# Optimization experiments

Hardware: AMD Instinct MI355X
Metric: run time of the kernel (lower is better)

Reference implementation:

```python
import jax, jax.numpy as jnp
import numpy as np

L_MAX = 3
MP_SCALING = 0.1
E = 640000
N_ATOMS = 20000
K = 32


def setup_inputs() -> dict:
    key = jax.random.key(0)
    k1, k2, k3, k4, k5 = jax.random.split(key, 5)
    sh = jax.random.normal(k1, (E, (L_MAX + 1) ** 2), dtype=jnp.float32)
    radial_basis = jax.random.normal(k2, (E, L_MAX + 1, K), dtype=jnp.float32)
    center_embedding = jax.random.normal(k3, (N_ATOMS, K), dtype=jnp.float32)
    centers = jax.random.randint(k4, (E,), 0, N_ATOMS, dtype=jnp.int32)
    neighbors = jax.random.randint(k5, (E,), 0, N_ATOMS, dtype=jnp.int32)
    return {
        "sh": sh,
        "radial_basis": radial_basis,
        "center_embedding": center_embedding,
        "centers": centers,
        "neighbors": neighbors,
        "n_atoms": N_ATOMS,
    }


def reference(sh, radial_basis, center_embedding, centers, neighbors, n_atoms):
    # Gather neighbor embeddings once: [E, K]
    emb_n = center_embedding[neighbors]
    blocks = []
    off = 0
    for l in range(L_MAX + 1):
        m = 2 * l + 1
        sh_l = sh[:, off:off + m]            # [E, m]
        off += m
        rb_l = radial_basis[:, l, :]          # [E, K]
        # edge-wise product sh * radial * gathered embedding: [E, m, K]
        src = sh_l[:, :, None] * (rb_l * emb_n)[:, None, :]
        # scatter-add over center atoms -> per-atom density [n_atoms, m, K]
        dens_l = jax.ops.segment_sum(src, centers, num_segments=n_atoms)
        blocks.append(dens_l * MP_SCALING)
    # concatenate per-l blocks along the component axis: [n_atoms, sum(2l+1)=16, K]
    return jnp.concatenate(blocks, axis=1)
```

## Files before the change

kernel.cpp:

```cpp
#include <hip/hip_runtime.h>

#define KDIM 32
#define CAP 160

__global__ void scatter_slots_kernel(const int* __restrict__ centers,
                                     const int* __restrict__ neighbors,
                                     int* __restrict__ cursor,
                                     int2* __restrict__ recs, int n) {
    int i = blockIdx.x * blockDim.x + threadIdx.x;
    if (i < n) {
        int c  = centers[i];
        int nn = neighbors[i];
        int pos = atomicAdd(&cursor[c], 1);
        if (pos < CAP) recs[(size_t)c * CAP + pos] = make_int2(i, nn);
    }
}


#define EDGE_BODY(EB, RP, SHP)                                            \
    {                                                                     \
        float t0 = RP[0 * KDIM + k] * EB;                                 \
        float t1 = RP[1 * KDIM + k] * EB;                                 \
        float t2 = RP[2 * KDIM + k] * EB;                                 \
        float t3 = RP[3 * KDIM + k] * EB;                                 \
        float4 sA = SHP[0];                                               \
        float4 sB = SHP[1];                                               \
        float c0 = hb ? t2 : t0;                                          \
        float c1 = hb ? t3 : t1;                                          \
        float c2 = hb ? t3 : t2;                                          \
        a0 += sA.x * c0;                                                  \
        a1 += sA.y * c1;                                                  \
        a2 += sA.z * c1;                                                  \
        a3 += sA.w * c1;                                                  \
        a4 += sB.x * c2;                                                  \
        a5 += sB.y * c2;                                                  \
        a6 += sB.z * c2;                                                  \
        a7 += sB.w * c2;                                                  \
    }

__global__ __launch_bounds__(256) void imp_main_kernel(
    const float* __restrict__ sh, const float* __restrict__ rb,
    const float* __restrict__ emb, const int2* __restrict__ recs,
    const int* __restrict__ cursor, float* __restrict__ out, int n_atoms) {
    int wid  = threadIdx.x >> 6;
    int aib  = wid >> 1;
    int half = wid & 1;
    int atom = blockIdx.x * 2 + aib;
    int lane = threadIdx.x & 63;
    int k = lane & 31;
    int h = lane >> 5;
    bool hb = (h != 0);

    __shared__ float red[2][8 * 64];

    float a0 = 0.f, a1 = 0.f, a2 = 0.f, a3 = 0.f;
    float a4 = 0.f, a5 = 0.f, a6 = 0.f, a7 = 0.f;

    bool valid = (atom < n_atoms);
    int i = 0, lim = 0;
    size_t base = (size_t)atom * CAP;
    if (valid) {
        int cnt = cursor[atom];
        if (cnt > CAP) cnt = CAP;
        int mid = (cnt + 1) >> 1;
        i   = half ? mid : 0;
        lim = half ? cnt : mid;
    }
    const int2* rbase = recs + base;

    for (; i + 4 <= lim; i += 4) {
        int2 r0 = rbase[i + 0];
        int2 r1 = rbase[i + 1];
        int2 r2 = rbase[i + 2];
        int2 r3 = rbase[i + 3];
        int e0 = __builtin_amdgcn_readfirstlane(r0.x);
        int n0 = __builtin_amdgcn_readfirstlane(r0.y);
        int e1 = __builtin_amdgcn_readfirstlane(r1.x);
        int n1 = __builtin_amdgcn_readfirstlane(r1.y);
        int e2 = __builtin_amdgcn_readfirstlane(r2.x);
        int n2 = __builtin_amdgcn_readfirstlane(r2.y);
        int e3 = __builtin_amdgcn_readfirstlane(r3.x);
        int n3 = __builtin_amdgcn_readfirstlane(r3.y);

        float eb0 = emb[(size_t)n0 * KDIM + k];
        float eb1 = emb[(size_t)n1 * KDIM + k];
        float eb2 = emb[(size_t)n2 * KDIM + k];
        float eb3 = emb[(size_t)n3 * KDIM + k];

        const float* rp0 = rb + (size_t)e0 * (4 * KDIM);
        const float* rp1 = rb + (size_t)e1 * (4 * KDIM);
        const float* rp2 = rb + (size_t)e2 * (4 * KDIM);
        const float* rp3 = rb + (size_t)e3 * (4 * KDIM);

        const float4* sp0 = (const float4*)(sh + (size_t)e0 * 16 + 8 * h);
        const float4* sp1 = (const float4*)(sh + (size_t)e1 * 16 + 8 * h);
        const float4* sp2 = (const float4*)(sh + (size_t)e2 * 16 + 8 * h);
        const float4* sp3 = (const float4*)(sh + (size_t)e3 * 16 + 8 * h);

        EDGE_BODY(eb0, rp0, sp0)
        EDGE_BODY(eb1, rp1, sp1)
        EDGE_BODY(eb2, rp2, sp2)
        EDGE_BODY(eb3, rp3, sp3)
    }
    for (; i < lim; i++) {
        int2 r0 = rbase[i];
        int e0 = __builtin_amdgcn_readfirstlane(r0.x);
        int n0 = __builtin_amdgcn_readfirstlane(r0.y);
        float eb0 = emb[(size_t)n0 * KDIM + k];
        const float* rp0 = rb + (size_t)e0 * (4 * KDIM);
        const float4* sp0 = (const float4*)(sh + (size_t)e0 * 16 + 8 * h);
        EDGE_BODY(eb0, rp0, sp0)
    }

    if (half) {
        float* rp = &red[aib][0];
        rp[0 * 64 + lane] = a0;
        rp[1 * 64 + lane] = a1;
        rp[2 * 64 + lane] = a2;
        rp[3 * 64 + lane] = a3;
        rp[4 * 64 + lane] = a4;
        rp[5 * 64 + lane] = a5;
        rp[6 * 64 + lane] = a6;
        rp[7 * 64 + lane] = a7;
    }
    __syncthreads();
    if (!half && valid) {
        const float* rp = &red[aib][0];
        a0 += rp[0 * 64 + lane];
        a1 += rp[1 * 64 + lane];
        a2 += rp[2 * 64 + lane];
        a3 += rp[3 * 64 + lane];
        a4 += rp[4 * 64 + lane];
        a5 += rp[5 * 64 + lane];
        a6 += rp[6 * 64 + lane];
        a7 += rp[7 * 64 + lane];

        const float SCALE = 0.1f;
        float* op = out + (size_t)atom * (16 * KDIM) + (size_t)(8 * h) * KDIM + k;
        op[0 * KDIM] = a0 * SCALE;
        op[1 * KDIM] = a1 * SCALE;
        op[2 * KDIM] = a2 * SCALE;
        op[3 * KDIM] = a3 * SCALE;
        op[4 * KDIM] = a4 * SCALE;
        op[5 * KDIM] = a5 * SCALE;
        op[6 * KDIM] = a6 * SCALE;
        op[7 * KDIM] = a7 * SCALE;
    }
}

extern "C" void kernel_launch(void* const* d_in, const int* in_sizes, int n_in,
                              void* d_out, int out_size, void* d_ws, size_t ws_size,
                              hipStream_t stream) {
    const float* sh        = (const float*)d_in[0];
    const float* rb        = (const float*)d_in[1];
    const float* emb       = (const float*)d_in[2];
    const int*   centers   = (const int*)d_in[3];
    const int*   neighbors = (const int*)d_in[4];

    int E = in_sizes[3];
    int N = in_sizes[2] / KDIM;

    float* out = (float*)d_out;

    int2* recs   = (int2*)d_ws;
    int*  cursor = (int*)(recs + (size_t)N * CAP);

    hipMemsetAsync(cursor, 0, (size_t)N * sizeof(int), stream);

    scatter_slots_kernel<<<(E + 255) / 256, 256, 0, stream>>>(centers, neighbors,
                                                              cursor, recs, E);

    int blocks = (N + 1) / 2;
    imp_main_kernel<<<blocks, 256, 0, stream>>>(sh, rb, emb, recs, cursor, out, N);
}
```

Measured before the change: 550.6 us.

## Use one wave per atom with lane-loaded edge records and readlane broadcast

```diff
diff --git a/kernel.cpp b/kernel.cpp
--- a/kernel.cpp
+++ b/kernel.cpp
@@ -38,71 +38,70 @@
         a7 += sB.w * c2;                                                  \
     }
 
+#define GROUP4(E0, N0, E1, N1, E2, N2, E3, N3)                            \
+    {                                                                     \
+        float eb0 = emb[(size_t)(N0) * KDIM + k];                         \
+        float eb1 = emb[(size_t)(N1) * KDIM + k];                         \
+        float eb2 = emb[(size_t)(N2) * KDIM + k];                         \
+        float eb3 = emb[(size_t)(N3) * KDIM + k];                         \
+        const float* rp0 = rb + (size_t)(E0) * (4 * KDIM);                \
+        const float* rp1 = rb + (size_t)(E1) * (4 * KDIM);                \
+        const float* rp2 = rb + (size_t)(E2) * (4 * KDIM);                \
+        const float* rp3 = rb + (size_t)(E3) * (4 * KDIM);                \
+        const float4* sp0 = (const float4*)(sh + (size_t)(E0) * 16 + 8 * h); \
+        const float4* sp1 = (const float4*)(sh + (size_t)(E1) * 16 + 8 * h); \
+        const float4* sp2 = (const float4*)(sh + (size_t)(E2) * 16 + 8 * h); \
+        const float4* sp3 = (const float4*)(sh + (size_t)(E3) * 16 + 8 * h); \
+        EDGE_BODY(eb0, rp0, sp0)                                          \
+        EDGE_BODY(eb1, rp1, sp1)                                          \
+        EDGE_BODY(eb2, rp2, sp2)                                          \
+        EDGE_BODY(eb3, rp3, sp3)                                          \
+    }
+
+#define RL(x, j) __builtin_amdgcn_readlane((x), (j))
+
 __global__ __launch_bounds__(256) void imp_main_kernel(
     const float* __restrict__ sh, const float* __restrict__ rb,
     const float* __restrict__ emb, const int2* __restrict__ recs,
     const int* __restrict__ cursor, float* __restrict__ out, int n_atoms) {
-    int wid  = threadIdx.x >> 6;
-    int aib  = wid >> 1;
-    int half = wid & 1;
-    int atom = blockIdx.x * 2 + aib;
+    int wave = (blockIdx.x * blockDim.x + threadIdx.x) >> 6;
     int lane = threadIdx.x & 63;
+    if (wave >= n_atoms) return;
     int k = lane & 31;
     int h = lane >> 5;
     bool hb = (h != 0);
 
-    __shared__ float red[2][8 * 64];
+    int cnt = cursor[wave];
+    if (cnt > CAP) cnt = CAP;
+    const int2* rbase = recs + (size_t)wave * CAP;
 
     float a0 = 0.f, a1 = 0.f, a2 = 0.f, a3 = 0.f;
     float a4 = 0.f, a5 = 0.f, a6 = 0.f, a7 = 0.f;
 
-    bool valid = (atom < n_atoms);
-    int i = 0, lim = 0;
-    size_t base = (size_t)atom * CAP;
-    if (valid) {
-        int cnt = cursor[atom];
-        if (cnt > CAP) cnt = CAP;
-        int mid = (cnt + 1) >> 1;
-        i   = half ? mid : 0;
-        lim = half ? cnt : mid;
+    int l8 = lane & 7;
+    int i = 0;
+    int2 cur = make_int2(0, 0);
+    if (cnt >= 8) cur = rbase[l8];
+    while (i + 8 <= cnt) {
+        int2 nxt = cur;
+        if (i + 16 <= cnt) nxt = rbase[i + 8 + l8];
+
+        int e0 = RL(cur.x, 0), n0 = RL(cur.y, 0);
+        int e1 = RL(cur.x, 1), n1 = RL(cur.y, 1);
+        int e2 = RL(cur.x, 2), n2 = RL(cur.y, 2);
+        int e3 = RL(cur.x, 3), n3 = RL(cur.y, 3);
+        int e4 = RL(cur.x, 4), n4 = RL(cur.y, 4);
+        int e5 = RL(cur.x, 5), n5 = RL(cur.y, 5);
+        int e6 = RL(cur.x, 6), n6 = RL(cur.y, 6);
+        int e7 = RL(cur.x, 7), n7 = RL(cur.y, 7);
+
+        GROUP4(e0, n0, e1, n1, e2, n2, e3, n3)
+        GROUP4(e4, n4, e5, n5, e6, n6, e7, n7)
+
+        cur = nxt;
+        i += 8;
     }
-    const int2* rbase = recs + base;
-
-    for (; i + 4 <= lim; i += 4) {
-        int2 r0 = rbase[i + 0];
-        int2 r1 = rbase[i + 1];
-        int2 r2 = rbase[i + 2];
-        int2 r3 = rbase[i + 3];
-        int e0 = __builtin_amdgcn_readfirstlane(r0.x);
-        int n0 = __builtin_amdgcn_readfirstlane(r0.y);
-        int e1 = __builtin_amdgcn_readfirstlane(r1.x);
-        int n1 = __builtin_amdgcn_readfirstlane(r1.y);
-        int e2 = __builtin_amdgcn_readfirstlane(r2.x);
-        int n2 = __builtin_amdgcn_readfirstlane(r2.y);
-        int e3 = __builtin_amdgcn_readfirstlane(r3.x);
-        int n3 = __builtin_amdgcn_readfirstlane(r3.y);
-
-        float eb0 = emb[(size_t)n0 * KDIM + k];
-        float eb1 = emb[(size_t)n1 * KDIM + k];
-        float eb2 = emb[(size_t)n2 * KDIM + k];
-        float eb3 = emb[(size_t)n3 * KDIM + k];
-
-        const float* rp0 = rb + (size_t)e0 * (4 * KDIM);
-        const float* rp1 = rb + (size_t)e1 * (4 * KDIM);
-        const float* rp2 = rb + (size_t)e2 * (4 * KDIM);
-        const float* rp3 = rb + (size_t)e3 * (4 * KDIM);
-
-        const float4* sp0 = (const float4*)(sh + (size_t)e0 * 16 + 8 * h);
-        const float4* sp1 = (const float4*)(sh + (size_t)e1 * 16 + 8 * h);
-        const float4* sp2 = (const float4*)(sh + (size_t)e2 * 16 + 8 * h);
-        const float4* sp3 = (const float4*)(sh + (size_t)e3 * 16 + 8 * h);
-
-        EDGE_BODY(eb0, rp0, sp0)
-        EDGE_BODY(eb1, rp1, sp1)
-        EDGE_BODY(eb2, rp2, sp2)
-        EDGE_BODY(eb3, rp3, sp3)
-    }
-    for (; i < lim; i++) {
+    for (; i < cnt; i++) {
         int2 r0 = rbase[i];
         int e0 = __builtin_amdgcn_readfirstlane(r0.x);
         int n0 = __builtin_amdgcn_readfirstlane(r0.y);
@@ -112,40 +111,16 @@
         EDGE_BODY(eb0, rp0, sp0)
     }
 
-    if (half) {
-        float* rp = &red[aib][0];
-        rp[0 * 64 + lane] = a0;
-        rp[1 * 64 + lane] = a1;
-        rp[2 * 64 + lane] = a2;
-        rp[3 * 64 + lane] = a3;
-        rp[4 * 64 + lane] = a4;
-        rp[5 * 64 + lane] = a5;
-        rp[6 * 64 + lane] = a6;
-        rp[7 * 64 + lane] = a7;
-    }
-    __syncthreads();
-    if (!half && valid) {
-        const float* rp = &red[aib][0];
-        a0 += rp[0 * 64 + lane];
-        a1 += rp[1 * 64 + lane];
-        a2 += rp[2 * 64 + lane];
-        a3 += rp[3 * 64 + lane];
-        a4 += rp[4 * 64 + lane];
-        a5 += rp[5 * 64 + lane];
-        a6 += rp[6 * 64 + lane];
-        a7 += rp[7 * 64 + lane];
-
-        const float SCALE = 0.1f;
-        float* op = out + (size_t)atom * (16 * KDIM) + (size_t)(8 * h) * KDIM + k;
-        op[0 * KDIM] = a0 * SCALE;
-        op[1 * KDIM] = a1 * SCALE;
-        op[2 * KDIM] = a2 * SCALE;
-        op[3 * KDIM] = a3 * SCALE;
-        op[4 * KDIM] = a4 * SCALE;
-        op[5 * KDIM] = a5 * SCALE;
-        op[6 * KDIM] = a6 * SCALE;
-        op[7 * KDIM] = a7 * SCALE;
-    }
+    const float SCALE = 0.1f;
+    float* op = out + (size_t)wave * (16 * KDIM) + (size_t)(8 * h) * KDIM + k;
+    op[0 * KDIM] = a0 * SCALE;
+    op[1 * KDIM] = a1 * SCALE;
+    op[2 * KDIM] = a2 * SCALE;
+    op[3 * KDIM] = a3 * SCALE;
+    op[4 * KDIM] = a4 * SCALE;
+    op[5 * KDIM] = a5 * SCALE;
+    op[6 * KDIM] = a6 * SCALE;
+    op[7 * KDIM] = a7 * SCALE;
 }
 
 extern "C" void kernel_launch(void* const* d_in, const int* in_sizes, int n_in,
@@ -170,6 +145,6 @@
     scatter_slots_kernel<<<(E + 255) / 256, 256, 0, stream>>>(centers, neighbors,
                                                               cursor, recs, E);
 
-    int blocks = (N + 1) / 2;
+    int blocks = (N * 64 + 255) / 256;
     imp_main_kernel<<<blocks, 256, 0, stream>>>(sh, rb, emb, recs, cursor, out, N);
 }
```

New measurement: 547.4 us, median of 2. Within noise of the previous version (-0.6%).
